# Performance work log

Measured on AMD Instinct MI355X. Metric: run time of the kernel, lower is better.

The kernel has to match this reference:

```python
import jax, jax.numpy as jnp
import numpy as np

N_HEAD = 16
CHUNK_SIZE = 64
TOP_B = 8
LOCAL_WINDOW = 256


def _l2_normalize(x, eps=1e-12):
    # matches torch F.normalize(dim=-1): x / max(||x||, eps)
    n = jnp.sqrt(jnp.sum(x * x, axis=-1, keepdims=True))
    return x / jnp.maximum(n, eps)


def setup_inputs() -> dict:
    key = jax.random.key(0)
    ks = jax.random.split(key, 9)
    B, T, C = 2, 2048, 1024
    s = lambda fan_in: 1.0 / np.sqrt(fan_in)
    return {
        "x": jax.random.normal(ks[0], (B, T, C), jnp.float32),
        "Wqkv": jax.random.normal(ks[1], (C, 3 * C), jnp.float32) * s(C),
        "bqkv": jax.random.normal(ks[2], (3 * C,), jnp.float32) * 0.02,
        "Wproj": jax.random.normal(ks[3], (C, C), jnp.float32) * s(C),
        "bproj": jax.random.normal(ks[4], (C,), jnp.float32) * 0.02,
        "Wrouter": jax.random.normal(ks[5], (C, 32), jnp.float32) * s(C),
        "brouter": jax.random.normal(ks[6], (32,), jnp.float32) * 0.02,
        "Wq_rt": jax.random.normal(ks[7], (C, 32), jnp.float32) * s(C),
        "bq_rt": jax.random.normal(ks[8], (32,), jnp.float32) * 0.02,
    }


def reference(x, Wqkv, bqkv, Wproj, bproj, Wrouter, brouter, Wq_rt, bq_rt):
    B, T, C = x.shape
    H = N_HEAD
    D = C // H

    # --- qkv projection ---
    qkv = x @ Wqkv + bqkv                       # [B,T,3C]
    q, k, v = jnp.split(qkv, 3, axis=-1)
    q = q.reshape(B, T, H, D).transpose(0, 2, 1, 3)  # [B,H,T,D]
    k = k.reshape(B, T, H, D).transpose(0, 2, 1, 3)
    v = v.reshape(B, T, H, D).transpose(0, 2, 1, 3)

    # --- routing (T > local_window + chunk_size) ---
    num_chunks = T // CHUNK_SIZE                 # T divisible -> no padding, mask all-True
    chunk_means = x.reshape(B, num_chunks, CHUNK_SIZE, C).mean(axis=2)  # [B,N,C]
    routing_embeds = chunk_means @ Wrouter + brouter                     # [B,N,32]
    q_rt = _l2_normalize(x @ Wq_rt + bq_rt)                              # [B,T,32]
    re_n = _l2_normalize(routing_embeds)
    routing_scores = jnp.einsum('btd,bnd->btn', q_rt, re_n)              # [B,T,N]
    _, chunk_indices = jax.lax.top_k(routing_scores, TOP_B)              # [B,T,top_b]

    # --- dense causal attention (forward path uses is_causal SDPA) ---
    scale = 1.0 / jnp.sqrt(jnp.asarray(D, x.dtype))
    scores = jnp.einsum('bhqd,bhkd->bhqk', q, k) * scale                 # [B,H,T,T]
    causal = jnp.tril(jnp.ones((T, T), dtype=bool))
    scores = jnp.where(causal[None, None], scores, -jnp.inf)
    attn = jax.nn.softmax(scores, axis=-1)
    y = jnp.einsum('bhqk,bhkd->bhqd', attn, v)                           # [B,H,T,D]
    y = y.transpose(0, 2, 1, 3).reshape(B, T, C)
    y = y @ Wproj + bproj

    return y, chunk_indices, routing_scores, routing_embeds
```

## Files before the change

kernel.cpp:

```cpp
#include <hip/hip_runtime.h>
#include <hip/hip_bf16.h>
#include <math.h>

#define B_   2
#define T_   2048
#define C_   1024
#define H_   16
#define D_   64
#define NCH  32
#define RD   32
#define TOPB 8

typedef __attribute__((ext_vector_type(8))) short bf16x8;
typedef __attribute__((ext_vector_type(4))) float f32x4;

static __device__ __forceinline__ unsigned short f2b(float f) {
    return __bfloat16_as_ushort(__float2bfloat16(f));
}

__global__ __launch_bounds__(256) void cast_bf16_kernel(
    const float* __restrict__ in, unsigned short* __restrict__ out, int n8)
{
    const int i = blockIdx.x * blockDim.x + threadIdx.x;
    if (i >= n8) return;
    float4 a = ((const float4*)in)[i * 2];
    float4 b = ((const float4*)in)[i * 2 + 1];
    bf16x8 o;
    o[0] = (short)f2b(a.x); o[1] = (short)f2b(a.y);
    o[2] = (short)f2b(a.z); o[3] = (short)f2b(a.w);
    o[4] = (short)f2b(b.x); o[5] = (short)f2b(b.y);
    o[6] = (short)f2b(b.z); o[7] = (short)f2b(b.w);
    *(bf16x8*)&out[i * 8] = o;
}

__global__ __launch_bounds__(256) void transpose_cast_kernel(
    const float* __restrict__ W, unsigned short* __restrict__ Wt, int K, int N)
{
    __shared__ float t[64][65];
    const int tid = threadIdx.x;
    const int n0 = blockIdx.x * 64, k0 = blockIdx.y * 64;
#pragma unroll
    for (int i = 0; i < 4; i++) {
        const int f = tid + i * 256;
        const int r = f >> 4, c4 = (f & 15) * 4;
        float4 v = *(const float4*)&W[(size_t)(k0 + r) * N + n0 + c4];
        t[r][c4 + 0] = v.x; t[r][c4 + 1] = v.y;
        t[r][c4 + 2] = v.z; t[r][c4 + 3] = v.w;
    }
    __syncthreads();
#pragma unroll
    for (int i = 0; i < 2; i++) {
        const int s = tid + i * 256;
        const int rn = s >> 3, ck8 = (s & 7) * 8;
        bf16x8 o;
#pragma unroll
        for (int j = 0; j < 8; j++) o[j] = (short)f2b(t[ck8 + j][rn]);
        *(bf16x8*)&Wt[(size_t)(n0 + rn) * K + k0 + ck8] = o;
    }
}

__global__ __launch_bounds__(512, 1) void gemm_qkv_256(
    const unsigned short* __restrict__ A, const unsigned short* __restrict__ Bt,
    const float* __restrict__ bias,
    unsigned short* __restrict__ qp, unsigned short* __restrict__ kp,
    unsigned short* __restrict__ vp, int M, int N, int K)
{
    __shared__ unsigned short lds[3][2][8192];

    const int tid  = threadIdx.x;
    const int wid  = tid >> 6;
    const int lane = tid & 63;
    const int lr = lane & 15, lg = lane >> 4;
    const int wm = wid >> 2, wn = wid & 3;

    const int bid = blockIdx.x;
    const int swz = (bid & 7) * 24 + (bid >> 3);
    const int m0 = (swz & 15) << 8;
    const int n0 = (swz >> 4) << 8;

    const int srow = tid >> 2;
    const int sswz = (((srow & 3) ^ ((srow >> 2) & 3)) << 4);
    const int skel = (((tid & 3) << 4) ^ sswz) >> 1;
    const unsigned short* gA0 = A  + (size_t)(m0 + srow) * K + skel;
    const unsigned short* gA1 = A  + (size_t)(m0 + srow + 128) * K + skel;
    const unsigned short* gB0 = Bt + (size_t)(n0 + srow) * K + skel;
    const unsigned short* gB1 = Bt + (size_t)(n0 + srow + 128) * K + skel;
    const int lb0 = (wid * 64) * 8;
    const int lb1 = (wid * 64 + 512) * 8;

#define QSTAGE(sl, kofs)                                                          \
    __builtin_amdgcn_global_load_lds(                                             \
        (const __attribute__((address_space(1))) int*)(gA0 + (kofs)),             \
        (__attribute__((address_space(3))) int*)&lds[sl][0][lb0], 16, 0, 0);      \
    __builtin_amdgcn_global_load_lds(                                             \
        (const __attribute__((address_space(1))) int*)(gA1 + (kofs)),             \
        (__attribute__((address_space(3))) int*)&lds[sl][0][lb1], 16, 0, 0);      \
    __builtin_amdgcn_global_load_lds(                                             \
        (const __attribute__((address_space(1))) int*)(gB0 + (kofs)),             \
        (__attribute__((address_space(3))) int*)&lds[sl][1][lb0], 16, 0, 0);      \
    __builtin_amdgcn_global_load_lds(                                             \
        (const __attribute__((address_space(1))) int*)(gB1 + (kofs)),             \
        (__attribute__((address_space(3))) int*)&lds[sl][1][lb1], 16, 0, 0);

    const int rswz = (((lr & 3) ^ ((lr >> 2) & 3)) << 4);
    const int acol = (((lg << 4) ^ rswz) >> 1);

    f32x4 acc[8][4];
#pragma unroll
    for (int i = 0; i < 8; i++)
#pragma unroll
        for (int j = 0; j < 4; j++) acc[i][j] = (f32x4){0.f, 0.f, 0.f, 0.f};

    const int nt = K >> 5;

    QSTAGE(0, 0)
    QSTAGE(1, 32)
    asm volatile("s_waitcnt vmcnt(4)" ::: "memory");
    __builtin_amdgcn_s_barrier();

    int cur = 0;
    for (int t = 0; t < nt; ++t) {
        int s2 = cur + 2; if (s2 >= 3) s2 -= 3;
        if (t + 2 < nt) { QSTAGE(s2, (t + 2) << 5) }

        const unsigned short* sA = &lds[cur][0][0];
        const unsigned short* sB = &lds[cur][1][0];

        bf16x8 bfr[4];
#pragma unroll
        for (int ni = 0; ni < 4; ni++)
            bfr[ni] = *(const bf16x8*)&sB[(wn * 64 + ni * 16 + lr) * 32 + acol];

        __builtin_amdgcn_s_setprio(1);
#pragma unroll
        for (int mi = 0; mi < 8; mi++) {
            bf16x8 af = *(const bf16x8*)&sA[(wm * 128 + mi * 16 + lr) * 32 + acol];
#pragma unroll
            for (int ni = 0; ni < 4; ni++)
                acc[mi][ni] = __builtin_amdgcn_mfma_f32_16x16x32_bf16(
                    af, bfr[ni], acc[mi][ni], 0, 0, 0);
        }
        __builtin_amdgcn_s_setprio(0);

        if (t + 1 < nt) {
            if (t + 2 < nt) { asm volatile("s_waitcnt vmcnt(4)" ::: "memory"); }
            else            { asm volatile("s_waitcnt vmcnt(0)" ::: "memory"); }
            __builtin_amdgcn_s_barrier();
        }
        cur += 1; if (cur == 3) cur = 0;
    }
#undef QSTAGE

#pragma unroll
    for (int ni = 0; ni < 4; ni++) {
        const int col = n0 + wn * 64 + ni * 16 + lr;
        const float bv = bias[col];
        const int which = col >> 10;
        const int c  = col & 1023;
        const int hh = c >> 6;
        const int dd = c & 63;
        unsigned short* dst = (which == 0) ? qp : (which == 1) ? kp : vp;
#pragma unroll
        for (int mi = 0; mi < 8; mi++) {
#pragma unroll
            for (int r = 0; r < 4; r++) {
                const int row = m0 + wm * 128 + mi * 16 + lg * 4 + r;
                const int bb = row >> 11, tt = row & 2047;
                dst[(((size_t)bb * H_ + hh) * T_ + tt) * D_ + dd] =
                    f2b(acc[mi][ni][r] + bv);
            }
        }
    }
}

__global__ __launch_bounds__(256) void gemm_mfma_f32out(
    const unsigned short* __restrict__ A, const unsigned short* __restrict__ Bt,
    const float* __restrict__ bias, float* __restrict__ out, int M, int N, int K)
{
    __shared__ unsigned short As[2][128 * 32];
    __shared__ unsigned short Bs[2][128 * 32];

    const int tid  = threadIdx.x;
    const int lane = tid & 63;
    const int wave = tid >> 6;
    const int lr = lane & 15, lg = lane >> 4;
    const int wm = wave >> 1, wn = wave & 1;
    const int n0 = blockIdx.x * 128, m0 = blockIdx.y * 128;

    const int srow = tid >> 2;
    const int scol = (tid & 3) * 8;
    const unsigned short* ga = A  + (size_t)(m0 + srow) * K + scol;
    const unsigned short* gb = Bt + (size_t)(n0 + srow) * K + scol;
    const int ldst = (tid & 0xC0) * 8;

    f32x4 acc[4][4];
#pragma unroll
    for (int i = 0; i < 4; i++)
#pragma unroll
        for (int j = 0; j < 4; j++) acc[i][j] = (f32x4){0.f, 0.f, 0.f, 0.f};

#define GSTAGE(buf, k0)                                                        \
    _Pragma("unroll")                                                          \
    for (int i = 0; i < 2; i++) {                                              \
        __builtin_amdgcn_global_load_lds(                                      \
            (const __attribute__((address_space(1))) int*)(ga + (k0) + (size_t)i * 64 * K), \
            (__attribute__((address_space(3))) int*)&As[buf][i * 2048 + ldst], 16, 0, 0);   \
        __builtin_amdgcn_global_load_lds(                                      \
            (const __attribute__((address_space(1))) int*)(gb + (k0) + (size_t)i * 64 * K), \
            (__attribute__((address_space(3))) int*)&Bs[buf][i * 2048 + ldst], 16, 0, 0);   \
    }

    const int nt = K >> 5;
    GSTAGE(0, 0);
    __syncthreads();

    int cur = 0;
    for (int t = 0; t < nt; ++t) {
        if (t + 1 < nt) { GSTAGE(cur ^ 1, (t + 1) << 5); }

        bf16x8 af[4], bfr[4];
#pragma unroll
        for (int mi = 0; mi < 4; mi++)
            af[mi] = *(const bf16x8*)&As[cur][(wm * 64 + mi * 16 + lr) * 32 + lg * 8];
#pragma unroll
        for (int ni = 0; ni < 4; ni++)
            bfr[ni] = *(const bf16x8*)&Bs[cur][(wn * 64 + ni * 16 + lr) * 32 + lg * 8];
#pragma unroll
        for (int mi = 0; mi < 4; mi++)
#pragma unroll
            for (int ni = 0; ni < 4; ni++)
                acc[mi][ni] = __builtin_amdgcn_mfma_f32_16x16x32_bf16(
                    af[mi], bfr[ni], acc[mi][ni], 0, 0, 0);

        __syncthreads();
        cur ^= 1;
    }
#undef GSTAGE

#pragma unroll
    for (int ni = 0; ni < 4; ni++) {
        const int col = n0 + wn * 64 + ni * 16 + lr;
        const float bv = bias[col];
#pragma unroll
        for (int mi = 0; mi < 4; mi++) {
#pragma unroll
            for (int r = 0; r < 4; r++) {
                const int row = m0 + wm * 64 + mi * 16 + lg * 4 + r;
                out[(size_t)row * N + col] = acc[mi][ni][r] + bv;
            }
        }
    }
}

__global__ void chunk_mean_kernel(const float* __restrict__ x, float* __restrict__ cm)
{
    const int bc = blockIdx.x;
    const int b = bc >> 5, n = bc & 31;
    const int c = blockIdx.y * 256 + threadIdx.x;
    const float* xp = x + ((size_t)b * T_ + n * 64) * C_;
    float s = 0.f;
    for (int i = 0; i < 64; i++) s += xp[(size_t)i * C_ + c];
    cm[(size_t)bc * C_ + c] = s * (1.0f / 64.0f);
}

__global__ void rowgemm32(const float* __restrict__ A, const float* __restrict__ W,
                          const float* __restrict__ bias, float* __restrict__ dst,
                          int M, int normalize)
{
    const int row  = blockIdx.x * 8 + (threadIdx.x >> 5);
    const int lane = threadIdx.x & 31;
    if (row >= M) return;
    const float* a = A + (size_t)row * C_;
    float acc = 0.f;
    for (int k = 0; k < C_; k += 4) {
        float4 a4 = *(const float4*)&a[k];
        acc += a4.x * W[(k + 0) * RD + lane];
        acc += a4.y * W[(k + 1) * RD + lane];
        acc += a4.z * W[(k + 2) * RD + lane];
        acc += a4.w * W[(k + 3) * RD + lane];
    }
    acc += bias[lane];
    if (normalize) {
        float ss = acc * acc;
#pragma unroll
        for (int off = 16; off >= 1; off >>= 1) ss += __shfl_xor(ss, off, 32);
        acc = acc / fmaxf(sqrtf(ss), 1e-12f);
    }
    dst[(size_t)row * RD + lane] = acc;
}

__global__ void l2norm_rows(const float* __restrict__ src, float* __restrict__ dst, int M)
{
    const int row  = blockIdx.x * 8 + (threadIdx.x >> 5);
    const int lane = threadIdx.x & 31;
    if (row >= M) return;
    float v = src[(size_t)row * RD + lane];
    float ss = v * v;
#pragma unroll
    for (int off = 16; off >= 1; off >>= 1) ss += __shfl_xor(ss, off, 32);
    dst[(size_t)row * RD + lane] = v / fmaxf(sqrtf(ss), 1e-12f);
}

__global__ __launch_bounds__(256) void qrt_kernel(
    const float* __restrict__ x, const float* __restrict__ W,
    const float* __restrict__ bias, float* __restrict__ dst)
{
    __shared__ float part[8][4][32];
    const int r0 = blockIdx.x * 4;
    const int g = threadIdx.x >> 5;
    const int n = threadIdx.x & 31;

    const float* w  = W + (size_t)(g * 128) * RD + n;
    const float* a0 = x + (size_t)(r0 + 0) * C_ + g * 128;
    const float* a1 = x + (size_t)(r0 + 1) * C_ + g * 128;
    const float* a2 = x + (size_t)(r0 + 2) * C_ + g * 128;
    const float* a3 = x + (size_t)(r0 + 3) * C_ + g * 128;

    float acc0 = 0.f, acc1 = 0.f, acc2 = 0.f, acc3 = 0.f;
#pragma unroll 8
    for (int i = 0; i < 128; i += 4) {
        const float w0 = w[(i + 0) * RD];
        const float w1 = w[(i + 1) * RD];
        const float w2 = w[(i + 2) * RD];
        const float w3 = w[(i + 3) * RD];
        float4 x0 = *(const float4*)&a0[i];
        float4 x1 = *(const float4*)&a1[i];
        float4 x2 = *(const float4*)&a2[i];
        float4 x3 = *(const float4*)&a3[i];
        acc0 += x0.x * w0; acc0 += x0.y * w1; acc0 += x0.z * w2; acc0 += x0.w * w3;
        acc1 += x1.x * w0; acc1 += x1.y * w1; acc1 += x1.z * w2; acc1 += x1.w * w3;
        acc2 += x2.x * w0; acc2 += x2.y * w1; acc2 += x2.z * w2; acc2 += x2.w * w3;
        acc3 += x3.x * w0; acc3 += x3.y * w1; acc3 += x3.z * w2; acc3 += x3.w * w3;
    }
    part[g][0][n] = acc0;
    part[g][1][n] = acc1;
    part[g][2][n] = acc2;
    part[g][3][n] = acc3;
    __syncthreads();

    if (g < 4) {
        float s = part[0][g][n];
#pragma unroll
        for (int gg = 1; gg < 8; gg++) s += part[gg][g][n];
        s += bias[n];
        float ss = s * s;
#pragma unroll
        for (int off = 16; off >= 1; off >>= 1) ss += __shfl_xor(ss, off, 32);
        dst[(size_t)(r0 + g) * RD + n] = s / fmaxf(sqrtf(ss), 1e-12f);
    }
}

__global__ void scores_topk(const float* __restrict__ qrt, const float* __restrict__ ren,
                            float* __restrict__ sc_out, float* __restrict__ idx_out)
{
    const int row = blockIdx.x * 64 + threadIdx.x;
    if (row >= B_ * T_) return;
    const int b = row / T_;
    float q[RD];
#pragma unroll
    for (int i = 0; i < RD; i++) q[i] = qrt[(size_t)row * RD + i];
    const float* rb = ren + (size_t)b * NCH * RD;
    float s[NCH];
#pragma unroll 4
    for (int n = 0; n < NCH; n++) {
        float acc = 0.f;
#pragma unroll
        for (int i = 0; i < RD; i++) acc += q[i] * rb[n * RD + i];
        s[n] = acc;
        sc_out[(size_t)row * NCH + n] = acc;
    }
    unsigned mask = 0;
    for (int t = 0; t < TOPB; t++) {
        float best = -INFINITY;
        int bi = 0;
#pragma unroll
        for (int n = 0; n < NCH; n++) {
            const bool ok = !((mask >> n) & 1u) && (s[n] > best);
            if (ok) { best = s[n]; bi = n; }
        }
        mask |= (1u << bi);
        idx_out[(size_t)row * TOPB + t] = (float)bi;
    }
}

#define LSTR 68
#define SCALE2 0.18033688f

__global__ __launch_bounds__(256) void attn_mfma(
    const unsigned short* __restrict__ qg, const unsigned short* __restrict__ kg,
    const unsigned short* __restrict__ vg, unsigned short* __restrict__ y)
{
    const int bid = blockIdx.x;
    const int xcd = bid & 7;
    const int j   = bid >> 3;
    const int h   = xcd + 8 * (j & 1);
    const int b   = (j >> 1) & 1;
    const int qt  = 31 - (j >> 2);

    const int tid  = threadIdx.x;
    const int wave = tid >> 6;
    const int lane = tid & 63;
    const int lg = lane >> 4;
    const int lr = lane & 15;

    __shared__ short Ks[2][64][LSTR];
    __shared__ short Vt[2][64][LSTR];

    const size_t base = ((size_t)(b * H_ + h) * T_) * D_;

    bf16x8 qf0, qf1;
    {
        const short* qp = (const short*)qg + base + (size_t)(qt * 64 + wave * 16 + lr) * D_;
        qf0 = *(const bf16x8*)&qp[lg * 8];
        qf1 = *(const bf16x8*)&qp[32 + lg * 8];
    }

    const int srr = tid >> 2;
    const int sc0 = (tid & 3) * 16;
    const int vrp = tid & 31;
    const int vcg = tid >> 5;
    const int kv0   = 2 * vrp;
    const int vslot = ((kv0 >> 5) << 5) + (((kv0 >> 2) & 3) << 3) +
                      (((kv0 >> 4) & 1) << 2) + (kv0 & 3);

    bf16x8 kreg0, kreg1, vreg0, vreg1;

    float m_run = -INFINITY, l_run = 0.f;
    f32x4 oacc[4];
#pragma unroll
    for (int r = 0; r < 4; r++) oacc[r] = (f32x4){0.f, 0.f, 0.f, 0.f};
    const int qrow_g = qt * 64 + wave * 16 + lr;

    {
        const short* kp = (const short*)kg + base + (size_t)srr * D_ + sc0;
        kreg0 = *(const bf16x8*)kp;
        kreg1 = *(const bf16x8*)(kp + 8);
        const short* vp = (const short*)vg + base + (size_t)kv0 * D_ + vcg * 8;
        vreg0 = *(const bf16x8*)vp;
        vreg1 = *(const bf16x8*)(vp + D_);
    }
    {
        *(bf16x8*)&Ks[0][srr][sc0]     = kreg0;
        *(bf16x8*)&Ks[0][srr][sc0 + 8] = kreg1;
#pragma unroll
        for (int jj = 0; jj < 8; jj++) {
            const unsigned int dw = ((unsigned int)(unsigned short)vreg0[jj]) |
                                    (((unsigned int)(unsigned short)vreg1[jj]) << 16);
            *(unsigned int*)&Vt[0][vcg * 8 + jj][vslot] = dw;
        }
    }
    if (qt >= 1) {
        const short* kp = (const short*)kg + base + (size_t)(64 + srr) * D_ + sc0;
        kreg0 = *(const bf16x8*)kp;
        kreg1 = *(const bf16x8*)(kp + 8);
        const short* vp = (const short*)vg + base + (size_t)(64 + kv0) * D_ + vcg * 8;
        vreg0 = *(const bf16x8*)vp;
        vreg1 = *(const bf16x8*)(vp + D_);
    }
    __syncthreads();

    for (int kt = 0; kt <= qt; ++kt) {
        const int cur = kt & 1;

        if (kt < qt) {
            *(bf16x8*)&Ks[cur ^ 1][srr][sc0]     = kreg0;
            *(bf16x8*)&Ks[cur ^ 1][srr][sc0 + 8] = kreg1;
#pragma unroll
            for (int jj = 0; jj < 8; jj++) {
                const unsigned int dw = ((unsigned int)(unsigned short)vreg0[jj]) |
                                        (((unsigned int)(unsigned short)vreg1[jj]) << 16);
                *(unsigned int*)&Vt[cur ^ 1][vcg * 8 + jj][vslot] = dw;
            }
        }
        if (kt + 2 <= qt) {
            const short* kp = (const short*)kg + base + (size_t)((kt + 2) * 64 + srr) * D_ + sc0;
            kreg0 = *(const bf16x8*)kp;
            kreg1 = *(const bf16x8*)(kp + 8);
            const short* vp = (const short*)vg + base + (size_t)((kt + 2) * 64 + kv0) * D_ + vcg * 8;
            vreg0 = *(const bf16x8*)vp;
            vreg1 = *(const bf16x8*)(vp + D_);
        }

        f32x4 s[4];
        __builtin_amdgcn_s_setprio(1);
#pragma unroll
        for (int cb = 0; cb < 4; cb++) {
            bf16x8 kf0 = *(const bf16x8*)&Ks[cur][cb * 16 + lr][lg * 8];
            bf16x8 kf1 = *(const bf16x8*)&Ks[cur][cb * 16 + lr][32 + lg * 8];
            f32x4 acc = (f32x4){0.f, 0.f, 0.f, 0.f};
            acc = __builtin_amdgcn_mfma_f32_16x16x32_bf16(kf0, qf0, acc, 0, 0, 0);
            acc = __builtin_amdgcn_mfma_f32_16x16x32_bf16(kf1, qf1, acc, 0, 0, 0);
            s[cb] = acc;
        }
        __builtin_amdgcn_s_setprio(0);

        if (kt == qt) {
#pragma unroll
            for (int cb = 0; cb < 4; cb++) {
#pragma unroll
                for (int r = 0; r < 4; r++) {
                    float sv = s[cb][r] * SCALE2;
                    if (kt * 64 + cb * 16 + lg * 4 + r > qrow_g) sv = -INFINITY;
                    s[cb][r] = sv;
                }
            }
        } else {
#pragma unroll
            for (int cb = 0; cb < 4; cb++)
#pragma unroll
                for (int r = 0; r < 4; r++) s[cb][r] *= SCALE2;
        }

        float rm = -INFINITY;
#pragma unroll
        for (int cb = 0; cb < 4; cb++)
#pragma unroll
            for (int r = 0; r < 4; r++) rm = fmaxf(rm, s[cb][r]);
        rm = fmaxf(rm, __shfl_xor(rm, 16));
        rm = fmaxf(rm, __shfl_xor(rm, 32));

        if (!__all(rm <= m_run + 8.0f)) {
            const float mnew = fmaxf(m_run, rm);
            const float fsc  = exp2f(m_run - mnew);
            m_run = mnew;
            l_run *= fsc;
            float fr[4];
#pragma unroll
            for (int r = 0; r < 4; r++) fr[r] = __shfl(fsc, lg * 4 + r);
#pragma unroll
            for (int db = 0; db < 4; db++)
#pragma unroll
                for (int r = 0; r < 4; r++) oacc[db][r] *= fr[r];
        }

        float p[4][4];
        float rs = 0.f;
#pragma unroll
        for (int cb = 0; cb < 4; cb++)
#pragma unroll
            for (int r = 0; r < 4; r++) {
                const float pv = exp2f(s[cb][r] - m_run);
                p[cb][r] = pv;
                rs += pv;
            }
        rs += __shfl_xor(rs, 16);
        rs += __shfl_xor(rs, 32);
        l_run += rs;

        bf16x8 pf0, pf1;
#pragma unroll
        for (int r = 0; r < 4; r++) {
            pf0[r]     = (short)f2b(p[0][r]);
            pf0[4 + r] = (short)f2b(p[1][r]);
            pf1[r]     = (short)f2b(p[2][r]);
            pf1[4 + r] = (short)f2b(p[3][r]);
        }

        __builtin_amdgcn_s_setprio(1);
#pragma unroll
        for (int db = 0; db < 4; db++) {
            bf16x8 vf0 = *(const bf16x8*)&Vt[cur][db * 16 + lr][lg * 8];
            bf16x8 vf1 = *(const bf16x8*)&Vt[cur][db * 16 + lr][32 + lg * 8];
            oacc[db] = __builtin_amdgcn_mfma_f32_16x16x32_bf16(pf0, vf0, oacc[db], 0, 0, 0);
            oacc[db] = __builtin_amdgcn_mfma_f32_16x16x32_bf16(pf1, vf1, oacc[db], 0, 0, 0);
        }
        __builtin_amdgcn_s_setprio(0);

        __syncthreads();
    }

#pragma unroll
    for (int r = 0; r < 4; r++) {
        const float lrow = __shfl(l_run, lg * 4 + r);
        const float inv = 1.0f / lrow;
        const int trow = qt * 64 + wave * 16 + lg * 4 + r;
        unsigned short* yp = y + (size_t)(b * T_ + trow) * C_ + h * D_;
#pragma unroll
        for (int db = 0; db < 4; db++)
            yp[db * 16 + lr] = f2b(oacc[db][r] * inv);
    }
}

extern "C" void kernel_launch(void* const* d_in, const int* in_sizes, int n_in,
                              void* d_out, int out_size, void* d_ws, size_t ws_size,
                              hipStream_t stream)
{
    const float* x       = (const float*)d_in[0];
    const float* Wqkv    = (const float*)d_in[1];
    const float* bqkv    = (const float*)d_in[2];
    const float* Wproj   = (const float*)d_in[3];
    const float* bproj   = (const float*)d_in[4];
    const float* Wrouter = (const float*)d_in[5];
    const float* brouter = (const float*)d_in[6];
    const float* Wq_rt   = (const float*)d_in[7];
    const float* bq_rt   = (const float*)d_in[8];

    float* out = (float*)d_out;
    char*  ws  = (char*)d_ws;

    const size_t MT  = (size_t)B_ * T_;
    const size_t QKV = MT * C_;

    unsigned short* xb   = (unsigned short*)ws;
    unsigned short* Wqt  = xb  + QKV;
    unsigned short* Wpt  = Wqt + (size_t)3 * C_ * C_;
    unsigned short* q    = Wpt + (size_t)C_ * C_;
    unsigned short* k    = q + QKV;
    unsigned short* v    = k + QKV;
    unsigned short* yab  = v + QKV;
    float* cm   = (float*)(yab + QKV);
    float* qrt  = cm  + (size_t)B_ * NCH * C_;
    float* ren  = qrt + MT * RD;

    float* y_out   = out;
    float* idx_out = out + QKV;
    float* sc_out  = idx_out + MT * TOPB;
    float* emb_out = sc_out + MT * NCH;

    cast_bf16_kernel<<<(int)(QKV / 8 / 256), 256, 0, stream>>>(x, xb, (int)(QKV / 8));
    transpose_cast_kernel<<<dim3(3 * C_ / 64, C_ / 64), 256, 0, stream>>>(Wqkv, Wqt, C_, 3 * C_);
    transpose_cast_kernel<<<dim3(C_ / 64, C_ / 64), 256, 0, stream>>>(Wproj, Wpt, C_, C_);

    gemm_qkv_256<<<dim3(192), 512, 0, stream>>>(
        xb, Wqt, bqkv, q, k, v, (int)MT, 3 * C_, C_);

    chunk_mean_kernel<<<dim3(B_ * NCH, 4), 256, 0, stream>>>(x, cm);
    rowgemm32<<<(B_ * NCH + 7) / 8, 256, 0, stream>>>(cm, Wrouter, brouter, emb_out, B_ * NCH, 0);
    l2norm_rows<<<(B_ * NCH + 7) / 8, 256, 0, stream>>>(emb_out, ren, B_ * NCH);
    qrt_kernel<<<(int)(MT / 4), 256, 0, stream>>>(x, Wq_rt, bq_rt, qrt);
    scores_topk<<<(int)(MT / 64), 64, 0, stream>>>(qrt, ren, sc_out, idx_out);

    attn_mfma<<<dim3(1024), 256, 0, stream>>>(q, k, v, yab);

    gemm_mfma_f32out<<<dim3(C_ / 128, MT / 128), 256, 0, stream>>>(
        yab, Wpt, bproj, y_out, (int)MT, C_, C_);
}
```

Measured before the change: 197.9 us.

## Fuse prep kernels, fold softmax scale into Q, streamline attention reductions

Merges the x cast, both weight transpose-casts, the q_rt projection and the chunk means into one multi-role launch, and fuses the router embedding with its L2 normalization. This removes several kernel launches. The attention scale is now applied to Q in the QKV GEMM epilogue instead of to every score tile. The attention kernel also uses tree-shaped max and sum reductions and a perm-based V transpose pack. Folding the scale before the bf16 rounding of Q slightly changes numerics.

```diff
diff --git a/kernel.cpp b/kernel.cpp
--- a/kernel.cpp
+++ b/kernel.cpp
@@ -18,45 +18,129 @@
     return __bfloat16_as_ushort(__float2bfloat16(f));
 }
 
-__global__ __launch_bounds__(256) void cast_bf16_kernel(
-    const float* __restrict__ in, unsigned short* __restrict__ out, int n8)
+#define SCALE2 0.18033688f
+
+__global__ __launch_bounds__(256) void prep_fused(
+    const float* __restrict__ x, unsigned short* __restrict__ xb,
+    const float* __restrict__ Wqkv, unsigned short* __restrict__ Wqt,
+    const float* __restrict__ Wproj, unsigned short* __restrict__ Wpt,
+    const float* __restrict__ Wq_rt, const float* __restrict__ bq_rt,
+    float* __restrict__ qrt, float* __restrict__ cm)
 {
-    const int i = blockIdx.x * blockDim.x + threadIdx.x;
-    if (i >= n8) return;
-    float4 a = ((const float4*)in)[i * 2];
-    float4 b = ((const float4*)in)[i * 2 + 1];
-    bf16x8 o;
-    o[0] = (short)f2b(a.x); o[1] = (short)f2b(a.y);
-    o[2] = (short)f2b(a.z); o[3] = (short)f2b(a.w);
-    o[4] = (short)f2b(b.x); o[5] = (short)f2b(b.y);
-    o[6] = (short)f2b(b.z); o[7] = (short)f2b(b.w);
-    *(bf16x8*)&out[i * 8] = o;
-}
-
-__global__ __launch_bounds__(256) void transpose_cast_kernel(
-    const float* __restrict__ W, unsigned short* __restrict__ Wt, int K, int N)
+    __shared__ float smem[64 * 65];
+    const int bid = blockIdx.x;
+    const int tid = threadIdx.x;
+
+    if (bid < 2048) {
+        const int i = bid * 256 + tid;
+        float4 a = ((const float4*)x)[i * 2];
+        float4 b = ((const float4*)x)[i * 2 + 1];
+        bf16x8 o;
+        o[0] = (short)f2b(a.x); o[1] = (short)f2b(a.y);
+        o[2] = (short)f2b(a.z); o[3] = (short)f2b(a.w);
+        o[4] = (short)f2b(b.x); o[5] = (short)f2b(b.y);
+        o[6] = (short)f2b(b.z); o[7] = (short)f2b(b.w);
+        *(bf16x8*)&xb[(size_t)i * 8] = o;
+    } else if (bid < 3072) {
+        const float* W; unsigned short* Wt; int N, local;
+        if (bid < 2816) { W = Wqkv;  Wt = Wqt; N = 3072; local = bid - 2048; }
+        else            { W = Wproj; Wt = Wpt; N = 1024; local = bid - 2816; }
+        const int nblk = N >> 6;
+        const int n0 = (local % nblk) * 64, k0 = (local / nblk) * 64;
+        float (*t)[65] = (float(*)[65])smem;
+#pragma unroll
+        for (int i = 0; i < 4; i++) {
+            const int f = tid + i * 256;
+            const int r = f >> 4, c4 = (f & 15) * 4;
+            float4 v = *(const float4*)&W[(size_t)(k0 + r) * N + n0 + c4];
+            t[r][c4 + 0] = v.x; t[r][c4 + 1] = v.y;
+            t[r][c4 + 2] = v.z; t[r][c4 + 3] = v.w;
+        }
+        __syncthreads();
+#pragma unroll
+        for (int i = 0; i < 2; i++) {
+            const int s = tid + i * 256;
+            const int rn = s >> 3, ck8 = (s & 7) * 8;
+            bf16x8 o;
+#pragma unroll
+            for (int j = 0; j < 8; j++) o[j] = (short)f2b(t[ck8 + j][rn]);
+            *(bf16x8*)&Wt[(size_t)(n0 + rn) * 1024 + k0 + ck8] = o;
+        }
+    } else if (bid < 4096) {
+        float (*part)[4][32] = (float(*)[4][32])smem;
+        const int r0 = (bid - 3072) * 4;
+        const int g = tid >> 5;
+        const int n = tid & 31;
+        const float* w  = Wq_rt + (size_t)(g * 128) * RD + n;
+        const float* a0 = x + (size_t)(r0 + 0) * C_ + g * 128;
+        const float* a1 = x + (size_t)(r0 + 1) * C_ + g * 128;
+        const float* a2 = x + (size_t)(r0 + 2) * C_ + g * 128;
+        const float* a3 = x + (size_t)(r0 + 3) * C_ + g * 128;
+        float acc0 = 0.f, acc1 = 0.f, acc2 = 0.f, acc3 = 0.f;
+#pragma unroll 8
+        for (int i = 0; i < 128; i += 4) {
+            const float w0 = w[(i + 0) * RD];
+            const float w1 = w[(i + 1) * RD];
+            const float w2 = w[(i + 2) * RD];
+            const float w3 = w[(i + 3) * RD];
+            float4 x0 = *(const float4*)&a0[i];
+            float4 x1 = *(const float4*)&a1[i];
+            float4 x2 = *(const float4*)&a2[i];
+            float4 x3 = *(const float4*)&a3[i];
+            acc0 += x0.x * w0; acc0 += x0.y * w1; acc0 += x0.z * w2; acc0 += x0.w * w3;
+            acc1 += x1.x * w0; acc1 += x1.y * w1; acc1 += x1.z * w2; acc1 += x1.w * w3;
+            acc2 += x2.x * w0; acc2 += x2.y * w1; acc2 += x2.z * w2; acc2 += x2.w * w3;
+            acc3 += x3.x * w0; acc3 += x3.y * w1; acc3 += x3.z * w2; acc3 += x3.w * w3;
+        }
+        part[g][0][n] = acc0;
+        part[g][1][n] = acc1;
+        part[g][2][n] = acc2;
+        part[g][3][n] = acc3;
+        __syncthreads();
+        if (g < 4) {
+            float s = part[0][g][n];
+#pragma unroll
+            for (int gg = 1; gg < 8; gg++) s += part[gg][g][n];
+            s += bq_rt[n];
+            float ss = s * s;
+#pragma unroll
+            for (int off = 16; off >= 1; off >>= 1) ss += __shfl_xor(ss, off, 32);
+            qrt[(size_t)(r0 + g) * RD + n] = s / fmaxf(sqrtf(ss), 1e-12f);
+        }
+    } else {
+        const int local = bid - 4096;
+        const int bc = local & 63;
+        const int b = bc >> 5, n = bc & 31;
+        const int c = (local >> 6) * 256 + tid;
+        const float* xp = x + ((size_t)b * T_ + n * 64) * C_;
+        float s = 0.f;
+        for (int i = 0; i < 64; i++) s += xp[(size_t)i * C_ + c];
+        cm[(size_t)bc * C_ + c] = s * (1.0f / 64.0f);
+    }
+}
+
+__global__ void embeds_kernel(const float* __restrict__ cm, const float* __restrict__ W,
+                              const float* __restrict__ bias,
+                              float* __restrict__ emb_out, float* __restrict__ ren)
 {
-    __shared__ float t[64][65];
-    const int tid = threadIdx.x;
-    const int n0 = blockIdx.x * 64, k0 = blockIdx.y * 64;
-#pragma unroll
-    for (int i = 0; i < 4; i++) {
-        const int f = tid + i * 256;
-        const int r = f >> 4, c4 = (f & 15) * 4;
-        float4 v = *(const float4*)&W[(size_t)(k0 + r) * N + n0 + c4];
-        t[r][c4 + 0] = v.x; t[r][c4 + 1] = v.y;
-        t[r][c4 + 2] = v.z; t[r][c4 + 3] = v.w;
-    }
-    __syncthreads();
-#pragma unroll
-    for (int i = 0; i < 2; i++) {
-        const int s = tid + i * 256;
-        const int rn = s >> 3, ck8 = (s & 7) * 8;
-        bf16x8 o;
-#pragma unroll
-        for (int j = 0; j < 8; j++) o[j] = (short)f2b(t[ck8 + j][rn]);
-        *(bf16x8*)&Wt[(size_t)(n0 + rn) * K + k0 + ck8] = o;
-    }
+    const int row  = blockIdx.x * 8 + (threadIdx.x >> 5);
+    const int lane = threadIdx.x & 31;
+    if (row >= B_ * NCH) return;
+    const float* a = cm + (size_t)row * C_;
+    float acc = 0.f;
+    for (int k = 0; k < C_; k += 4) {
+        float4 a4 = *(const float4*)&a[k];
+        acc += a4.x * W[(k + 0) * RD + lane];
+        acc += a4.y * W[(k + 1) * RD + lane];
+        acc += a4.z * W[(k + 2) * RD + lane];
+        acc += a4.w * W[(k + 3) * RD + lane];
+    }
+    acc += bias[lane];
+    emb_out[(size_t)row * RD + lane] = acc;
+    float ss = acc * acc;
+#pragma unroll
+    for (int off = 16; off >= 1; off >>= 1) ss += __shfl_xor(ss, off, 32);
+    ren[(size_t)row * RD + lane] = acc / fmaxf(sqrtf(ss), 1e-12f);
 }
 
 __global__ __launch_bounds__(512, 1) void gemm_qkv_256(
@@ -160,6 +244,7 @@
         const int hh = c >> 6;
         const int dd = c & 63;
         unsigned short* dst = (which == 0) ? qp : (which == 1) ? kp : vp;
+        const float postmul = (which == 0) ? SCALE2 : 1.0f;
 #pragma unroll
         for (int mi = 0; mi < 8; mi++) {
 #pragma unroll
@@ -167,7 +252,7 @@
                 const int row = m0 + wm * 128 + mi * 16 + lg * 4 + r;
                 const int bb = row >> 11, tt = row & 2047;
                 dst[(((size_t)bb * H_ + hh) * T_ + tt) * D_ + dd] =
-                    f2b(acc[mi][ni][r] + bv);
+                    f2b((acc[mi][ni][r] + bv) * postmul);
             }
         }
     }
@@ -252,104 +337,6 @@
     }
 }
 
-__global__ void chunk_mean_kernel(const float* __restrict__ x, float* __restrict__ cm)
-{
-    const int bc = blockIdx.x;
-    const int b = bc >> 5, n = bc & 31;
-    const int c = blockIdx.y * 256 + threadIdx.x;
-    const float* xp = x + ((size_t)b * T_ + n * 64) * C_;
-    float s = 0.f;
-    for (int i = 0; i < 64; i++) s += xp[(size_t)i * C_ + c];
-    cm[(size_t)bc * C_ + c] = s * (1.0f / 64.0f);
-}
-
-__global__ void rowgemm32(const float* __restrict__ A, const float* __restrict__ W,
-                          const float* __restrict__ bias, float* __restrict__ dst,
-                          int M, int normalize)
-{
-    const int row  = blockIdx.x * 8 + (threadIdx.x >> 5);
-    const int lane = threadIdx.x & 31;
-    if (row >= M) return;
-    const float* a = A + (size_t)row * C_;
-    float acc = 0.f;
-    for (int k = 0; k < C_; k += 4) {
-        float4 a4 = *(const float4*)&a[k];
-        acc += a4.x * W[(k + 0) * RD + lane];
-        acc += a4.y * W[(k + 1) * RD + lane];
-        acc += a4.z * W[(k + 2) * RD + lane];
-        acc += a4.w * W[(k + 3) * RD + lane];
-    }
-    acc += bias[lane];
-    if (normalize) {
-        float ss = acc * acc;
-#pragma unroll
-        for (int off = 16; off >= 1; off >>= 1) ss += __shfl_xor(ss, off, 32);
-        acc = acc / fmaxf(sqrtf(ss), 1e-12f);
-    }
-    dst[(size_t)row * RD + lane] = acc;
-}
-
-__global__ void l2norm_rows(const float* __restrict__ src, float* __restrict__ dst, int M)
-{
-    const int row  = blockIdx.x * 8 + (threadIdx.x >> 5);
-    const int lane = threadIdx.x & 31;
-    if (row >= M) return;
-    float v = src[(size_t)row * RD + lane];
-    float ss = v * v;
-#pragma unroll
-    for (int off = 16; off >= 1; off >>= 1) ss += __shfl_xor(ss, off, 32);
-    dst[(size_t)row * RD + lane] = v / fmaxf(sqrtf(ss), 1e-12f);
-}
-
-__global__ __launch_bounds__(256) void qrt_kernel(
-    const float* __restrict__ x, const float* __restrict__ W,
-    const float* __restrict__ bias, float* __restrict__ dst)
-{
-    __shared__ float part[8][4][32];
-    const int r0 = blockIdx.x * 4;
-    const int g = threadIdx.x >> 5;
-    const int n = threadIdx.x & 31;
-
-    const float* w  = W + (size_t)(g * 128) * RD + n;
-    const float* a0 = x + (size_t)(r0 + 0) * C_ + g * 128;
-    const float* a1 = x + (size_t)(r0 + 1) * C_ + g * 128;
-    const float* a2 = x + (size_t)(r0 + 2) * C_ + g * 128;
-    const float* a3 = x + (size_t)(r0 + 3) * C_ + g * 128;
-
-    float acc0 = 0.f, acc1 = 0.f, acc2 = 0.f, acc3 = 0.f;
-#pragma unroll 8
-    for (int i = 0; i < 128; i += 4) {
-        const float w0 = w[(i + 0) * RD];
-        const float w1 = w[(i + 1) * RD];
-        const float w2 = w[(i + 2) * RD];
-        const float w3 = w[(i + 3) * RD];
-        float4 x0 = *(const float4*)&a0[i];
-        float4 x1 = *(const float4*)&a1[i];
-        float4 x2 = *(const float4*)&a2[i];
-        float4 x3 = *(const float4*)&a3[i];
-        acc0 += x0.x * w0; acc0 += x0.y * w1; acc0 += x0.z * w2; acc0 += x0.w * w3;
-        acc1 += x1.x * w0; acc1 += x1.y * w1; acc1 += x1.z * w2; acc1 += x1.w * w3;
-        acc2 += x2.x * w0; acc2 += x2.y * w1; acc2 += x2.z * w2; acc2 += x2.w * w3;
-        acc3 += x3.x * w0; acc3 += x3.y * w1; acc3 += x3.z * w2; acc3 += x3.w * w3;
-    }
-    part[g][0][n] = acc0;
-    part[g][1][n] = acc1;
-    part[g][2][n] = acc2;
-    part[g][3][n] = acc3;
-    __syncthreads();
-
-    if (g < 4) {
-        float s = part[0][g][n];
-#pragma unroll
-        for (int gg = 1; gg < 8; gg++) s += part[gg][g][n];
-        s += bias[n];
-        float ss = s * s;
-#pragma unroll
-        for (int off = 16; off >= 1; off >>= 1) ss += __shfl_xor(ss, off, 32);
-        dst[(size_t)(r0 + g) * RD + n] = s / fmaxf(sqrtf(ss), 1e-12f);
-    }
-}
-
 __global__ void scores_topk(const float* __restrict__ qrt, const float* __restrict__ ren,
                             float* __restrict__ sc_out, float* __restrict__ idx_out)
 {
@@ -384,7 +371,6 @@
 }
 
 #define LSTR 68
-#define SCALE2 0.18033688f
 
 __global__ __launch_bounds__(256) void attn_mfma(
     const unsigned short* __restrict__ qg, const unsigned short* __restrict__ kg,
@@ -431,6 +417,18 @@
     for (int r = 0; r < 4; r++) oacc[r] = (f32x4){0.f, 0.f, 0.f, 0.f};
     const int qrow_g = qt * 64 + wave * 16 + lr;
 
+#define VPACK(buf)                                                              \
+    {                                                                           \
+        const unsigned* v0d = (const unsigned*)&vreg0;                          \
+        const unsigned* v1d = (const unsigned*)&vreg1;                          \
+        _Pragma("unroll")                                                       \
+        for (int jj = 0; jj < 8; jj++) {                                        \
+            const unsigned sel = (jj & 1) ? 0x07060302u : 0x05040100u;          \
+            const unsigned dw = __builtin_amdgcn_perm(v1d[jj >> 1], v0d[jj >> 1], sel); \
+            *(unsigned*)&Vt[buf][vcg * 8 + jj][vslot] = dw;                     \
+        }                                                                       \
+    }
+
     {
         const short* kp = (const short*)kg + base + (size_t)srr * D_ + sc0;
         kreg0 = *(const bf16x8*)kp;
@@ -442,12 +440,7 @@
     {
         *(bf16x8*)&Ks[0][srr][sc0]     = kreg0;
         *(bf16x8*)&Ks[0][srr][sc0 + 8] = kreg1;
-#pragma unroll
-        for (int jj = 0; jj < 8; jj++) {
-            const unsigned int dw = ((unsigned int)(unsigned short)vreg0[jj]) |
-                                    (((unsigned int)(unsigned short)vreg1[jj]) << 16);
-            *(unsigned int*)&Vt[0][vcg * 8 + jj][vslot] = dw;
-        }
+        VPACK(0)
     }
     if (qt >= 1) {
         const short* kp = (const short*)kg + base + (size_t)(64 + srr) * D_ + sc0;
@@ -465,12 +458,7 @@
         if (kt < qt) {
             *(bf16x8*)&Ks[cur ^ 1][srr][sc0]     = kreg0;
             *(bf16x8*)&Ks[cur ^ 1][srr][sc0 + 8] = kreg1;
-#pragma unroll
-            for (int jj = 0; jj < 8; jj++) {
-                const unsigned int dw = ((unsigned int)(unsigned short)vreg0[jj]) |
-                                        (((unsigned int)(unsigned short)vreg1[jj]) << 16);
-                *(unsigned int*)&Vt[cur ^ 1][vcg * 8 + jj][vslot] = dw;
-            }
+            VPACK(cur ^ 1)
         }
         if (kt + 2 <= qt) {
             const short* kp = (const short*)kg + base + (size_t)((kt + 2) * 64 + srr) * D_ + sc0;
@@ -496,26 +484,20 @@
 
         if (kt == qt) {
 #pragma unroll
-            for (int cb = 0; cb < 4; cb++) {
-#pragma unroll
-                for (int r = 0; r < 4; r++) {
-                    float sv = s[cb][r] * SCALE2;
-                    if (kt * 64 + cb * 16 + lg * 4 + r > qrow_g) sv = -INFINITY;
-                    s[cb][r] = sv;
-                }
-            }
-        } else {
-#pragma unroll
             for (int cb = 0; cb < 4; cb++)
 #pragma unroll
-                for (int r = 0; r < 4; r++) s[cb][r] *= SCALE2;
-        }
-
-        float rm = -INFINITY;
-#pragma unroll
-        for (int cb = 0; cb < 4; cb++)
-#pragma unroll
-            for (int r = 0; r < 4; r++) rm = fmaxf(rm, s[cb][r]);
+                for (int r = 0; r < 4; r++)
+                    if (kt * 64 + cb * 16 + lg * 4 + r > qrow_g) s[cb][r] = -INFINITY;
+        }
+
+        float rm;
+        {
+            const float t0 = fmaxf(fmaxf(s[0][0], s[0][1]), fmaxf(s[0][2], s[0][3]));
+            const float t1 = fmaxf(fmaxf(s[1][0], s[1][1]), fmaxf(s[1][2], s[1][3]));
+            const float t2 = fmaxf(fmaxf(s[2][0], s[2][1]), fmaxf(s[2][2], s[2][3]));
+            const float t3 = fmaxf(fmaxf(s[3][0], s[3][1]), fmaxf(s[3][2], s[3][3]));
+            rm = fmaxf(fmaxf(t0, t1), fmaxf(t2, t3));
+        }
         rm = fmaxf(rm, __shfl_xor(rm, 16));
         rm = fmaxf(rm, __shfl_xor(rm, 32));
 
@@ -534,15 +516,19 @@
         }
 
         float p[4][4];
-        float rs = 0.f;
 #pragma unroll
         for (int cb = 0; cb < 4; cb++)
 #pragma unroll
-            for (int r = 0; r < 4; r++) {
-                const float pv = exp2f(s[cb][r] - m_run);
-                p[cb][r] = pv;
-                rs += pv;
-            }
+            for (int r = 0; r < 4; r++)
+                p[cb][r] = exp2f(s[cb][r] - m_run);
+        float rs;
+        {
+            const float t0 = (p[0][0] + p[0][1]) + (p[0][2] + p[0][3]);
+            const float t1 = (p[1][0] + p[1][1]) + (p[1][2] + p[1][3]);
+            const float t2 = (p[2][0] + p[2][1]) + (p[2][2] + p[2][3]);
+            const float t3 = (p[3][0] + p[3][1]) + (p[3][2] + p[3][3]);
+            rs = (t0 + t1) + (t2 + t3);
+        }
         rs += __shfl_xor(rs, 16);
         rs += __shfl_xor(rs, 32);
         l_run += rs;
@@ -568,6 +554,7 @@
 
         __syncthreads();
     }
+#undef VPACK
 
 #pragma unroll
     for (int r = 0; r < 4; r++) {
@@ -617,17 +604,13 @@
     float* sc_out  = idx_out + MT * TOPB;
     float* emb_out = sc_out + MT * NCH;
 
-    cast_bf16_kernel<<<(int)(QKV / 8 / 256), 256, 0, stream>>>(x, xb, (int)(QKV / 8));
-    transpose_cast_kernel<<<dim3(3 * C_ / 64, C_ / 64), 256, 0, stream>>>(Wqkv, Wqt, C_, 3 * C_);
-    transpose_cast_kernel<<<dim3(C_ / 64, C_ / 64), 256, 0, stream>>>(Wproj, Wpt, C_, C_);
+    prep_fused<<<4352, 256, 0, stream>>>(x, xb, Wqkv, Wqt, Wproj, Wpt,
+                                         Wq_rt, bq_rt, qrt, cm);
 
     gemm_qkv_256<<<dim3(192), 512, 0, stream>>>(
         xb, Wqt, bqkv, q, k, v, (int)MT, 3 * C_, C_);
 
-    chunk_mean_kernel<<<dim3(B_ * NCH, 4), 256, 0, stream>>>(x, cm);
-    rowgemm32<<<(B_ * NCH + 7) / 8, 256, 0, stream>>>(cm, Wrouter, brouter, emb_out, B_ * NCH, 0);
-    l2norm_rows<<<(B_ * NCH + 7) / 8, 256, 0, stream>>>(emb_out, ren, B_ * NCH);
-    qrt_kernel<<<(int)(MT / 4), 256, 0, stream>>>(x, Wq_rt, bq_rt, qrt);
+    embeds_kernel<<<8, 256, 0, stream>>>(cm, Wrouter, brouter, emb_out, ren);
     scores_topk<<<(int)(MT / 64), 64, 0, stream>>>(qrt, ren, sc_out, idx_out);
 
     attn_mfma<<<dim3(1024), 256, 0, stream>>>(q, k, v, yab);
```

Measured after the change: 186.8 us. 5.6% less time.
